# Optimization experiments

Measured on AMD Instinct MI355X. Metric: run time of the kernel, lower is better.

Reference implementation:

```python
import math
import jax, jax.numpy as jnp
import numpy as np

FEAT = (32, 96, 96)   # feature-space D,H,W (image 128x384x384 at scale 4)
C_IN = 256
DIM = 48              # patch_dim
PS = 24               # patch_size = instance_crop_size // feature_scale
SIG = 1024
POS = (8, 8, 8, 4)    # pos_emb_shape
N = 64                # num instances
SCALE = 4
CROP = 96


def setup_inputs() -> dict:
    key = jax.random.key(0)
    ks = jax.random.split(key, 16)
    def w(k, shape, s=0.02):
        return jax.random.normal(k, shape, dtype=jnp.float32) * s
    feature = jax.random.normal(ks[0], FEAT + (C_IN,), dtype=jnp.float32)
    # locations in original-image pixel coordinates
    locations = jax.random.uniform(ks[1], (N, 3), dtype=jnp.float32) * jnp.asarray(
        [FEAT[0] * SCALE, FEAT[1] * SCALE, FEAT[2] * SCALE], jnp.float32)
    return dict(
        feature=feature, locations=locations,
        conv0_w=w(ks[2], (3, 3, 3, C_IN, DIM)), conv0_b=jnp.zeros((DIM,), jnp.float32),
        conv1_w=w(ks[3], (3, 3, 3, DIM, DIM)), conv1_b=jnp.zeros((DIM,), jnp.float32),
        ca_w=w(ks[4], (DIM, DIM)), ca_b=jnp.zeros((DIM,), jnp.float32),
        sig_w=w(ks[5], (4 * 4 * 4 * DIM, SIG)), sig_b=jnp.zeros((SIG,), jnp.float32),
        ln_scale=jnp.ones((SIG,), jnp.float32), ln_bias=jnp.zeros((SIG,), jnp.float32),
        pe1_w=w(ks[6], (SIG, SIG)), pe1_b=jnp.zeros((SIG,), jnp.float32),
        pe2_w=w(ks[7], (SIG, SIG)), pe2_b=jnp.zeros((SIG,), jnp.float32),
        pe3_w=w(ks[8], (SIG, math.prod(POS))), pe3_b=jnp.zeros((math.prod(POS),), jnp.float32),
        pe_proj_w=w(ks[9], (POS[-1], DIM)),
        ct_w=w(ks[10], (2, 2, 2, DIM, 1)), ct_b=jnp.zeros((1,), jnp.float32),
    )


def _conv3d(x, w, b):
    y = jax.lax.conv_general_dilated(x[None], w, (1, 1, 1), 'SAME',
        dimension_numbers=('NDHWC', 'DHWIO', 'NDHWC'))[0]
    return y + b


def _forward(feature, locations, conv0_w, conv0_b, conv1_w, conv1_b, ca_w, ca_b,
             sig_w, sig_b, ln_scale, ln_bias, pe1_w, pe1_b, pe2_w, pe2_b,
             pe3_w, pe3_b, pe_proj_w, ct_w, ct_b):
    n = locations.shape[0]
    locs = locations / SCALE
    # feature mixing convs
    x = jax.nn.gelu(_conv3d(feature, conv0_w, conv0_b))
    x = _conv3d(x, conv1_w, conv1_b)                       # [D,H,W,DIM]
    # _get_patch: gather PS^3 sub-volumes at N locations with bounds masking
    loc0 = locs.astype(jnp.int32) - PS // 2                 # [N,3] top-left corners
    grid = jnp.mgrid[:PS, :PS, :PS]                         # [3,PS,PS,PS]
    coords = grid[None] + loc0[:, :, None, None, None]      # [N,3,PS,PS,PS]
    limit = jnp.asarray(x.shape[:-1]).reshape(1, 3, 1, 1, 1)
    valid = (coords >= 0).all(axis=1) & (coords < limit).all(axis=1)  # [N,PS,PS,PS]
    patches = jnp.where(valid[..., None],
                        x[coords[:, 0], coords[:, 1], coords[:, 2]], 0.0)
    # ChannelAttention (SE-style: global pool -> dense -> sigmoid gate)
    gate = jax.nn.sigmoid(patches.mean(axis=(1, 2, 3)) @ ca_w + ca_b)  # [N,DIM]
    patches = patches * gate[:, None, None, None, :]
    # _get_signiture
    bw = PS // 4
    inner = patches[:, bw:-bw, bw:-bw, bw:-bw, :]
    s = jax.image.resize(inner, (n, 4, 4, 4, DIM), 'linear').reshape(n, -1)
    s = s @ sig_w + sig_b
    mu = s.mean(-1, keepdims=True)
    var = ((s - mu) ** 2).mean(-1, keepdims=True)
    patch_sigs = (s - mu) * jax.lax.rsqrt(var + 1e-6) * ln_scale + ln_bias
    # _add_pos_encoding
    p = jax.nn.gelu(patch_sigs @ pe1_w + pe1_b)
    p = jax.nn.gelu(p @ pe2_w + pe2_b)
    p = p @ pe3_w + pe3_b                                   # [N, prod(POS)]
    p = jax.image.resize(p.reshape(-1, *POS), (n, PS, PS, PS, POS[-1]), 'linear')
    patches = jax.nn.relu(patches + p @ pe_proj_w)          # [N,PS,PS,PS,DIM]
    # decode: ConvTranspose x2 then trilinear resize to full crop
    logits = jax.lax.conv_transpose(patches, ct_w, (2, 2, 2), 'SAME',
        dimension_numbers=('NDHWC', 'DHWIO', 'NDHWC')) + ct_b  # [N,2PS,2PS,2PS,1]
    logits = jax.image.resize(logits[..., 0], (n, CROP, CROP, CROP), 'linear')
    mask = locs[:, -1] >= 0
    plocs = jnp.where(mask[:, None], loc0 * SCALE, -1)
    return patch_sigs, logits, plocs[:, 0], plocs[:, 1], plocs[:, 2], mask


def reference(feature, locations, conv0_w, conv0_b, conv1_w, conv1_b, ca_w, ca_b,
              sig_w, sig_b, ln_scale, ln_bias, pe1_w, pe1_b, pe2_w, pe2_b,
              pe3_w, pe3_b, pe_proj_w, ct_w, ct_b):
    return _forward(feature, locations, conv0_w, conv0_b, conv1_w, conv1_b, ca_w,
                    ca_b, sig_w, sig_b, ln_scale, ln_bias, pe1_w, pe1_b, pe2_w,
                    pe2_b, pe3_w, pe3_b, pe_proj_w, ct_w, ct_b)
```

## Files before the change

kernel.cpp:

```cpp
#include <hip/hip_runtime.h>
#include <hip/hip_bf16.h>
#include <math.h>


#define NLOC 64

typedef __attribute__((ext_vector_type(8))) short short8_t;
typedef __attribute__((ext_vector_type(4))) float f32x4;

__device__ __forceinline__ float gelu_f(float x) {
    return 0.5f * x * (1.0f + tanhf(0.7978845608028654f * (x + 0.044715f * x * x * x)));
}

__device__ __forceinline__ short f2bf(float x) {
    union { __hip_bfloat16 h; short s; } u;
    u.h = __float2bfloat16(x);
    return u.s;
}

__device__ __forceinline__ float bf2f(short s) {
    union { unsigned u; float f; } u;
    u.u = ((unsigned)(unsigned short)s) << 16;
    return u.f;
}

__constant__ float W12c[4][12] = {
    {0.25f, 0.375f, 0.25f, 0.125f, 0.f, 0.f, 0.f, 0.f, 0.f, 0.f, 0.f, 0.f},
    {0.f, 0.f, 1.f/9.f, 2.f/9.f, 1.f/3.f, 2.f/9.f, 1.f/9.f, 0.f, 0.f, 0.f, 0.f, 0.f},
    {0.f, 0.f, 0.f, 0.f, 0.f, 1.f/9.f, 2.f/9.f, 1.f/3.f, 2.f/9.f, 1.f/9.f, 0.f, 0.f},
    {0.f, 0.f, 0.f, 0.f, 0.f, 0.f, 0.f, 0.f, 0.125f, 0.25f, 0.375f, 0.25f}};

__device__ __forceinline__ void up_w(int i, float ratio, int inmax,
                                     int& j0, int& j1, float& w0, float& w1) {
    float c = ((float)i + 0.5f) * ratio - 0.5f;
    float fj = floorf(c);
    float f = c - fj;
    int jj = (int)fj;
    j0 = min(max(jj, 0), inmax);
    j1 = min(max(jj + 1, 0), inmax);
    w0 = 1.f - f;
    w1 = f;
}

__global__ void prep_w0_kernel(const float* __restrict__ w0, short* __restrict__ wf) {
    const int tid = blockIdx.x * 256 + threadIdx.x;
    if (tid >= 27 * 8 * 3 * 64) return;
    const int lane = tid & 63;
    const int t2 = tid >> 6;
    const int nt = t2 % 3;
    const int t3 = t2 / 3;
    const int kk = t3 & 7, tap = t3 >> 3;
    const int g = lane >> 4, rr = lane & 15;
    const int co = nt * 16 + rr;
    short8_t frag;
#pragma unroll
    for (int e = 0; e < 8; e++) {
        const int ci = kk * 32 + g * 8 + e;
        frag[e] = f2bf(w0[((long)(tap * 256 + ci)) * 48 + co]);
    }
    ((short8_t*)wf)[tid] = frag;
}

__global__ void prep_w1_kernel(const float* __restrict__ w1, short* __restrict__ wf) {
    const int tid = blockIdx.x * 256 + threadIdx.x;
    if (tid >= 27 * 2 * 3 * 64) return;
    const int lane = tid & 63;
    const int t2 = tid >> 6;
    const int nt = t2 % 3;
    const int t3 = t2 / 3;
    const int kk = t3 & 1, tap = t3 >> 1;
    const int g = lane >> 4, rr = lane & 15;
    const int co = nt * 16 + rr;
    short8_t frag;
#pragma unroll
    for (int e = 0; e < 8; e++) {
        const int ci = kk * 32 + g * 8 + e;
        frag[e] = (ci < 48) ? f2bf(w1[((long)(tap * 48 + ci)) * 48 + co]) : (short)0;
    }
    ((short8_t*)wf)[tid] = frag;
}

#define HV 600
#define HSTR 40

__global__ __launch_bounds__(256) void conv0_mfma(const float* __restrict__ feat,
                                                  const short* __restrict__ wf,
                                                  const float* __restrict__ bias,
                                                  short* __restrict__ x0b) {
    __shared__ short slds[HV * HSTR];
    const int tid = threadIdx.x;
    const int lane = tid & 63, wid = tid >> 6;
    const int g = lane >> 4, r = lane & 15;
    const int bz = blockIdx.x / 144, by = (blockIdx.x / 12) % 12, bx = blockIdx.x % 12;
    const int z0 = bz * 4, y0 = by * 8, x0c = bx * 8;
    int h0[4];
#pragma unroll
    for (int mt = 0; mt < 4; mt++) {
        const int t = wid * 64 + mt * 16 + r;
        h0[mt] = ((t >> 6) * 10 + ((t >> 3) & 7)) * 10 + (t & 7);
    }
    f32x4 acc[4][3];
#pragma unroll
    for (int mt = 0; mt < 4; mt++)
#pragma unroll
        for (int nt = 0; nt < 3; nt++) acc[mt][nt] = (f32x4){0.f, 0.f, 0.f, 0.f};
    const short8_t zfrag = {0, 0, 0, 0, 0, 0, 0, 0};
    const short8_t* wf8 = (const short8_t*)wf;

    for (int kk = 0; kk < 8; kk++) {
        __syncthreads();
        for (int h = tid; h < HV; h += 256) {
            const int hx = h % 10, hy = (h / 10) % 10, hz = h / 100;
            const int zz = z0 + hz - 1, yy = y0 + hy - 1, xx = x0c + hx - 1;
            short8_t s8[4];
            if ((unsigned)zz < 32u && (unsigned)yy < 96u && (unsigned)xx < 96u) {
                const float4* src =
                    (const float4*)(feat + (((((long)zz * 96 + yy) * 96 + xx)) << 8) + kk * 32);
#pragma unroll
                for (int q = 0; q < 4; q++) {
                    const float4 a = src[2 * q], b = src[2 * q + 1];
                    s8[q][0] = f2bf(a.x); s8[q][1] = f2bf(a.y);
                    s8[q][2] = f2bf(a.z); s8[q][3] = f2bf(a.w);
                    s8[q][4] = f2bf(b.x); s8[q][5] = f2bf(b.y);
                    s8[q][6] = f2bf(b.z); s8[q][7] = f2bf(b.w);
                }
            } else {
#pragma unroll
                for (int q = 0; q < 4; q++) s8[q] = zfrag;
            }
            short8_t* dst = (short8_t*)(slds + h * HSTR);
#pragma unroll
            for (int q = 0; q < 4; q++) dst[q] = s8[q];
        }
        __syncthreads();
        for (int tap = 0; tap < 27; tap++) {
            const int dh = (tap / 9) * 100 + ((tap / 3) % 3) * 10 + (tap % 3);
            short8_t bfr[3];
#pragma unroll
            for (int nt = 0; nt < 3; nt++)
                bfr[nt] = wf8[(size_t)tap * 1536 + kk * 192 + nt * 64 + lane];
            short8_t afr[4];
#pragma unroll
            for (int mt = 0; mt < 4; mt++)
                afr[mt] = *(const short8_t*)(slds + (h0[mt] + dh) * HSTR + g * 8);
#pragma unroll
            for (int mt = 0; mt < 4; mt++)
#pragma unroll
                for (int nt = 0; nt < 3; nt++)
                    acc[mt][nt] = __builtin_amdgcn_mfma_f32_16x16x32_bf16(afr[mt], bfr[nt],
                                                                          acc[mt][nt], 0, 0, 0);
        }
    }
#pragma unroll
    for (int nt = 0; nt < 3; nt++) {
        const int co = nt * 16 + r;
        const float bv = bias[co];
#pragma unroll
        for (int mt = 0; mt < 4; mt++) {
#pragma unroll
            for (int rg = 0; rg < 4; rg++) {
                const int t = wid * 64 + mt * 16 + g * 4 + rg;
                const int z = z0 + (t >> 6), y = y0 + ((t >> 3) & 7), x = x0c + (t & 7);
                const long gi = ((long)z * 96 + y) * 96 + x;
                x0b[gi * 48 + co] = f2bf(gelu_f(acc[mt][nt][rg] + bv));
            }
        }
    }
}

#define C1ROW 48

__global__ __launch_bounds__(256, 1) void conv1_mfma_b(const short* __restrict__ x0b,
                                                       const short* __restrict__ wf,
                                                       const float* __restrict__ bias,
                                                       short* __restrict__ x1b) {
    __shared__ short slds[HV * C1ROW];
    const int tid = threadIdx.x;
    const int lane = tid & 63, wid = tid >> 6;
    const int g = lane >> 4, r = lane & 15;
    const int bz = blockIdx.x / 144, by = (blockIdx.x / 12) % 12, bx = blockIdx.x % 12;
    const int z0 = bz * 4, y0 = by * 8, x0c = bx * 8;
    int h0[4];
#pragma unroll
    for (int mt = 0; mt < 4; mt++) {
        const int t = wid * 64 + mt * 16 + r;
        h0[mt] = ((t >> 6) * 10 + ((t >> 3) & 7)) * 10 + (t & 7);
    }
    f32x4 acc[4][3];
#pragma unroll
    for (int mt = 0; mt < 4; mt++)
#pragma unroll
        for (int nt = 0; nt < 3; nt++) acc[mt][nt] = (f32x4){0.f, 0.f, 0.f, 0.f};
    const short8_t zfrag = {0, 0, 0, 0, 0, 0, 0, 0};
    const short8_t* wf8 = (const short8_t*)wf;

    for (int h = tid; h < HV; h += 256) {
        const int hx = h % 10, hy = (h / 10) % 10, hz = h / 100;
        const int zz = z0 + hz - 1, yy = y0 + hy - 1, xx = x0c + hx - 1;
        short8_t s8[6];
        if ((unsigned)zz < 32u && (unsigned)yy < 96u && (unsigned)xx < 96u) {
            const short8_t* src = (const short8_t*)(x0b + (((long)zz * 96 + yy) * 96 + xx) * 48);
#pragma unroll
            for (int q = 0; q < 6; q++) s8[q] = src[q];
        } else {
#pragma unroll
            for (int q = 0; q < 6; q++) s8[q] = zfrag;
        }
        short8_t* dst = (short8_t*)(slds + h * C1ROW);
#pragma unroll
        for (int q = 0; q < 6; q++) dst[q] = s8[q];
    }
    __syncthreads();

    for (int tap = 0; tap < 27; tap++) {
        const int dh = (tap / 9) * 100 + ((tap / 3) % 3) * 10 + (tap % 3);
#pragma unroll
        for (int kk = 0; kk < 2; kk++) {
            short8_t bfr[3];
#pragma unroll
            for (int nt = 0; nt < 3; nt++)
                bfr[nt] = wf8[(size_t)tap * 384 + kk * 192 + nt * 64 + lane];
            short8_t afr[4];
#pragma unroll
            for (int mt = 0; mt < 4; mt++) {
                afr[mt] = zfrag;
                if (!(kk == 1 && g >= 2))
                    afr[mt] =
                        *(const short8_t*)(slds + (h0[mt] + dh) * C1ROW + kk * 32 + g * 8);
            }
#pragma unroll
            for (int mt = 0; mt < 4; mt++)
#pragma unroll
                for (int nt = 0; nt < 3; nt++)
                    acc[mt][nt] = __builtin_amdgcn_mfma_f32_16x16x32_bf16(afr[mt], bfr[nt],
                                                                          acc[mt][nt], 0, 0, 0);
        }
    }
#pragma unroll
    for (int nt = 0; nt < 3; nt++) {
        const int co = nt * 16 + r;
        const float bv = bias[co];
#pragma unroll
        for (int mt = 0; mt < 4; mt++) {
#pragma unroll
            for (int rg = 0; rg < 4; rg++) {
                const int t = wid * 64 + mt * 16 + g * 4 + rg;
                const int z = z0 + (t >> 6), y = y0 + ((t >> 3) & 7), x = x0c + (t & 7);
                const long gi = ((long)z * 96 + y) * 96 + x;
                x1b[gi * 48 + co] = f2bf(acc[mt][nt][rg] + bv);
            }
        }
    }
}

__global__ __launch_bounds__(256) void mean_part_kernel(const short* __restrict__ x1b,
                                                        const float* __restrict__ locations,
                                                        float* __restrict__ part) {
    __shared__ float red[256];
    const int n = blockIdx.x, i = blockIdx.y;
    const int tid = threadIdx.x;
    const int ch = tid & 63, grp = tid >> 6;
    const int lz = (int)(locations[n * 3 + 0] * 0.25f) - 12;
    const int ly = (int)(locations[n * 3 + 1] * 0.25f) - 12;
    const int lx = (int)(locations[n * 3 + 2] * 0.25f) - 12;
    float acc = 0.f;
    const int z = lz + i;
    if (ch < 48 && (unsigned)z < 32u) {
        for (int p = grp; p < 576; p += 4) {
            const int j = p / 24, k = p % 24;
            const int y = ly + j, x = lx + k;
            if ((unsigned)y < 96u && (unsigned)x < 96u)
                acc += bf2f(x1b[(((long)z * 96 + y) * 96 + x) * 48 + ch]);
        }
    }
    red[tid] = acc;
    __syncthreads();
    if (tid < 48)
        part[(n * 24 + i) * 48 + tid] = red[tid] + red[tid + 64] + red[tid + 128] + red[tid + 192];
}

__global__ void gate_kernel(const float* __restrict__ part, const float* __restrict__ caw,
                            const float* __restrict__ cab, float* __restrict__ gate) {
    __shared__ float sm[48];
    const int n = blockIdx.x, t = threadIdx.x;
    if (t < 48) {
        float a = 0.f;
        for (int i = 0; i < 24; i++) a += part[(n * 24 + i) * 48 + t];
        sm[t] = a * (1.f / 13824.f);
    }
    __syncthreads();
    if (t < 48) {
        float g = cab[t];
        for (int c = 0; c < 48; c++) g += sm[c] * caw[c * 48 + t];
        gate[n * 48 + t] = 1.f / (1.f + expf(-g));
    }
}

__global__ __launch_bounds__(256) void rs1_kernel(const short* __restrict__ x1b,
                                                  const float* __restrict__ locations,
                                                  const float* __restrict__ gate,
                                                  float* __restrict__ t1) {
    const int idx = blockIdx.x * 256 + threadIdx.x;
    int ch = idx % 48;
    int r = idx / 48;
    int c4 = r & 3; r >>= 2;
    int j = r % 12; r /= 12;
    int i = r % 12;
    int n = r / 12;
    const int lz = (int)(locations[n * 3 + 0] * 0.25f) - 6;
    const int ly = (int)(locations[n * 3 + 1] * 0.25f) - 6;
    const int lx = (int)(locations[n * 3 + 2] * 0.25f) - 6;
    const int z = lz + i, y = ly + j;
    float acc = 0.f;
    if ((unsigned)z < 32u && (unsigned)y < 96u) {
        const short* row = x1b + (((long)z * 96 + y) * 96) * 48 + ch;
#pragma unroll
        for (int k = 0; k < 12; k++) {
            const int x = lx + k;
            if ((unsigned)x < 96u) acc += W12c[c4][k] * bf2f(row[(long)x * 48]);
        }
    }
    t1[idx] = acc * gate[n * 48 + ch];
}

__global__ __launch_bounds__(256) void rs2_kernel(const float* __restrict__ t1,
                                                  float* __restrict__ t2) {
    const int idx = blockIdx.x * 256 + threadIdx.x;
    int ch = idx % 48;
    int r = idx / 48;
    int c = r & 3; r >>= 2;
    int b = r & 3; r >>= 2;
    int i = r % 12;
    int n = r / 12;
    float acc = 0.f;
#pragma unroll
    for (int j = 0; j < 12; j++)
        acc += W12c[b][j] * t1[(((long)((n * 12 + i) * 12 + j) * 4 + c)) * 48 + ch];
    t2[idx] = acc;
}

__global__ __launch_bounds__(256) void rs3_kernel(const float* __restrict__ t2,
                                                  float* __restrict__ rs) {
    const int idx = blockIdx.x * 256 + threadIdx.x;
    int ch = idx % 48;
    int r = idx / 48;
    int c = r & 3; r >>= 2;
    int b = r & 3; r >>= 2;
    int a = r & 3;
    int n = r >> 2;
    float acc = 0.f;
#pragma unroll
    for (int i = 0; i < 12; i++)
        acc += W12c[a][i] * t2[(((long)((n * 12 + i) * 4 + b) * 4 + c)) * 48 + ch];
    rs[idx] = acc;
}

template <int K, bool GEL>
__global__ __launch_bounds__(256) void mlp_kernel(const float* __restrict__ A,
                                                  const float* __restrict__ W,
                                                  const float* __restrict__ bias,
                                                  float* __restrict__ C, int N) {
    const int n = threadIdx.x & 63;
    const int j = blockIdx.x * 4 + (threadIdx.x >> 6);
    float acc = bias[j];
    const float* a = A + (long)n * K;
    const float* wp = W + j;
    for (int k = 0; k < K; k++) acc += a[k] * wp[(long)k * N];
    if (GEL) acc = gelu_f(acc);
    C[(long)n * N + j] = acc;
}

__global__ __launch_bounds__(256) void ln_kernel(const float* __restrict__ s,
                                                 const float* __restrict__ sc,
                                                 const float* __restrict__ bi,
                                                 float* __restrict__ out) {
    __shared__ float red[256];
    const int n = blockIdx.x, tid = threadIdx.x;
    float4 v = ((const float4*)(s + (long)n * 1024))[tid];
    red[tid] = v.x + v.y + v.z + v.w;
    __syncthreads();
    for (int off = 128; off > 0; off >>= 1) {
        if (tid < off) red[tid] += red[tid + off];
        __syncthreads();
    }
    const float mu = red[0] * (1.f / 1024.f);
    __syncthreads();
    const float d0 = v.x - mu, d1 = v.y - mu, d2 = v.z - mu, d3 = v.w - mu;
    red[tid] = d0 * d0 + d1 * d1 + d2 * d2 + d3 * d3;
    __syncthreads();
    for (int off = 128; off > 0; off >>= 1) {
        if (tid < off) red[tid] += red[tid + off];
        __syncthreads();
    }
    const float rstd = rsqrtf(red[0] * (1.f / 1024.f) + 1e-6f);
    const int base = n * 1024 + tid * 4;
    out[base + 0] = d0 * rstd * sc[tid * 4 + 0] + bi[tid * 4 + 0];
    out[base + 1] = d1 * rstd * sc[tid * 4 + 1] + bi[tid * 4 + 1];
    out[base + 2] = d2 * rstd * sc[tid * 4 + 2] + bi[tid * 4 + 2];
    out[base + 3] = d3 * rstd * sc[tid * 4 + 3] + bi[tid * 4 + 3];
}

__global__ __launch_bounds__(256) void deconv_kernel(const short* __restrict__ x1b,
                                                     const float* __restrict__ locations,
                                                     const float* __restrict__ gate,
                                                     const float* __restrict__ p3,
                                                     const float* __restrict__ projw,
                                                     const float* __restrict__ ctw,
                                                     const float* __restrict__ ctb,
                                                     float* __restrict__ l48) {
    __shared__ float s_ctw[384], s_proj[192], s_gate[48];
    const int n = blockIdx.y, tid = threadIdx.x;
    for (int i = tid; i < 384; i += 256) s_ctw[i] = ctw[i];
    if (tid < 192) s_proj[tid] = projw[tid];
    if (tid < 48) s_gate[tid] = gate[n * 48 + tid];
    __syncthreads();
    const int vox = blockIdx.x * 256 + tid;
    const int q = vox % 24, pp = (vox / 24) % 24, m = vox / 576;
    const int lz = (int)(locations[n * 3 + 0] * 0.25f) - 12;
    const int ly = (int)(locations[n * 3 + 1] * 0.25f) - 12;
    const int lx = (int)(locations[n * 3 + 2] * 0.25f) - 12;
    const int z = lz + m, y = ly + pp, x = lx + q;
    float pf[48];
    const bool valid = (unsigned)z < 32u && (unsigned)y < 96u && (unsigned)x < 96u;
    if (valid) {
        const short8_t* src = (const short8_t*)(x1b + (((long)z * 96 + y) * 96 + x) * 48);
#pragma unroll
        for (int t8 = 0; t8 < 6; t8++) {
            const short8_t v = src[t8];
#pragma unroll
            for (int e = 0; e < 8; e++) pf[t8 * 8 + e] = bf2f(v[e]) * s_gate[t8 * 8 + e];
        }
    } else {
#pragma unroll
        for (int c = 0; c < 48; c++) pf[c] = 0.f;
    }
    int jz[2], jy[2], jx[2];
    float wz[2], wy[2], wx[2];
    const float r3 = 1.f / 3.f;
    up_w(m, r3, 7, jz[0], jz[1], wz[0], wz[1]);
    up_w(pp, r3, 7, jy[0], jy[1], wy[0], wy[1]);
    up_w(q, r3, 7, jx[0], jx[1], wx[0], wx[1]);
    const float4* prow = (const float4*)(p3 + (long)n * 2048);
    float prx = 0.f, pry = 0.f, prz = 0.f, prw = 0.f;
#pragma unroll
    for (int a = 0; a < 2; a++)
#pragma unroll
        for (int b = 0; b < 2; b++)
#pragma unroll
            for (int c = 0; c < 2; c++) {
                const float wgt = wz[a] * wy[b] * wx[c];
                float4 v = prow[(jz[a] * 8 + jy[b]) * 8 + jx[c]];
                prx += wgt * v.x;
                pry += wgt * v.y;
                prz += wgt * v.z;
                prw += wgt * v.w;
            }
#pragma unroll
    for (int c = 0; c < 48; c++) {
        float v = pf[c] + prx * s_proj[c] + pry * s_proj[48 + c] + prz * s_proj[96 + c] +
                  prw * s_proj[144 + c];
        pf[c] = fmaxf(v, 0.f);
    }
    const float bias = ctb[0];
#pragma unroll
    for (int a = 0; a < 2; a++)
#pragma unroll
        for (int b = 0; b < 2; b++)
#pragma unroll
            for (int c = 0; c < 2; c++) {
                const float* wrow = s_ctw + (((1 - a) * 2 + (1 - b)) * 2 + (1 - c)) * 48;
                float acc = bias;
#pragma unroll
                for (int ch = 0; ch < 48; ch++) acc += pf[ch] * wrow[ch];
                l48[(((long)n * 48 + 2 * m + a) * 48 + 2 * pp + b) * 48 + 2 * q + c] = acc;
            }
}

__global__ __launch_bounds__(256) void resize96_kernel(const float* __restrict__ l48,
                                                       float* __restrict__ out) {
    const int n = blockIdx.y;
    const int vox = blockIdx.x * 256 + threadIdx.x;
    const int kx = vox % 96, jy = (vox / 96) % 96, iz = vox / 9216;
    int a0, a1, b0, b1, c0, c1;
    float wa0, wa1, wb0, wb1, wc0, wc1;
    up_w(iz, 0.5f, 47, a0, a1, wa0, wa1);
    up_w(jy, 0.5f, 47, b0, b1, wb0, wb1);
    up_w(kx, 0.5f, 47, c0, c1, wc0, wc1);
    const float* base = l48 + (long)n * 110592;
    const float v =
        wa0 * (wb0 * (wc0 * base[(a0 * 48 + b0) * 48 + c0] + wc1 * base[(a0 * 48 + b0) * 48 + c1]) +
               wb1 * (wc0 * base[(a0 * 48 + b1) * 48 + c0] + wc1 * base[(a0 * 48 + b1) * 48 + c1])) +
        wa1 * (wb0 * (wc0 * base[(a1 * 48 + b0) * 48 + c0] + wc1 * base[(a1 * 48 + b0) * 48 + c1]) +
               wb1 * (wc0 * base[(a1 * 48 + b1) * 48 + c0] + wc1 * base[(a1 * 48 + b1) * 48 + c1]));
    out[(long)n * 884736 + vox] = v;
}

__global__ void tail_kernel(const float* __restrict__ locations, float* __restrict__ out) {
    const int n = threadIdx.x;
    if (n < NLOC) {
        const float l0 = locations[n * 3 + 0] * 0.25f;
        const float l1 = locations[n * 3 + 1] * 0.25f;
        const float l2 = locations[n * 3 + 2] * 0.25f;
        const int z = (int)l0 - 12, y = (int)l1 - 12, x = (int)l2 - 12;
        const bool mask = (l2 >= 0.f);
        out[n] = mask ? (float)(z * 4) : -1.f;
        out[64 + n] = mask ? (float)(y * 4) : -1.f;
        out[128 + n] = mask ? (float)(x * 4) : -1.f;
        out[192 + n] = mask ? 1.f : 0.f;
    }
}

static const size_t OFF_X0 = 0;
static const size_t OFF_X1 = 14155776;
static const size_t OFF_WF0 = 14155776;
static const size_t OFF_GATE = 4096;
static const size_t OFF_T1 = 8192;
static const size_t OFF_T2 = 1777664;
static const size_t OFF_RS = 2367488;
static const size_t OFF_S = 2564096;
static const size_t OFF_P1 = 2629632;
static const size_t OFF_P2 = 2695168;
static const size_t OFF_P3 = 2760704;
static const size_t OFF_L48 = 2891776;
static const size_t OFF_PART = 10000000;

static const size_t OUT_WF1 = 65536;

extern "C" void kernel_launch(void* const* d_in, const int* in_sizes, int n_in,
                              void* d_out, int out_size, void* d_ws, size_t ws_size,
                              hipStream_t stream) {
    const float* feature = (const float*)d_in[0];
    const float* locations = (const float*)d_in[1];
    const float* w0 = (const float*)d_in[2];
    const float* b0 = (const float*)d_in[3];
    const float* w1 = (const float*)d_in[4];
    const float* b1 = (const float*)d_in[5];
    const float* caw = (const float*)d_in[6];
    const float* cab = (const float*)d_in[7];
    const float* sigw = (const float*)d_in[8];
    const float* sigb = (const float*)d_in[9];
    const float* lnsc = (const float*)d_in[10];
    const float* lnbi = (const float*)d_in[11];
    const float* pe1w = (const float*)d_in[12];
    const float* pe1b = (const float*)d_in[13];
    const float* pe2w = (const float*)d_in[14];
    const float* pe2b = (const float*)d_in[15];
    const float* pe3w = (const float*)d_in[16];
    const float* pe3b = (const float*)d_in[17];
    const float* projw = (const float*)d_in[18];
    const float* ctw = (const float*)d_in[19];
    const float* ctb = (const float*)d_in[20];
    float* ws = (float*)d_ws;
    float* out = (float*)d_out;

    short* x0b = (short*)(ws + OFF_X0);
    short* x1b = (short*)(ws + OFF_X1);
    short* wf0 = (short*)(ws + OFF_WF0);
    short* wf1 = (short*)(out + OUT_WF1);

    prep_w0_kernel<<<162, 256, 0, stream>>>(w0, wf0);
    prep_w1_kernel<<<41, 256, 0, stream>>>(w1, wf1);

    conv0_mfma<<<1152, 256, 0, stream>>>(feature, wf0, b0, x0b);
    conv1_mfma_b<<<1152, 256, 0, stream>>>(x0b, wf1, b1, x1b);

    mean_part_kernel<<<dim3(64, 24), 256, 0, stream>>>(x1b, locations, ws + OFF_PART);
    gate_kernel<<<64, 64, 0, stream>>>(ws + OFF_PART, caw, cab, ws + OFF_GATE);

    rs1_kernel<<<6912, 256, 0, stream>>>(x1b, locations, ws + OFF_GATE, ws + OFF_T1);
    rs2_kernel<<<2304, 256, 0, stream>>>(ws + OFF_T1, ws + OFF_T2);
    rs3_kernel<<<768, 256, 0, stream>>>(ws + OFF_T2, ws + OFF_RS);

    mlp_kernel<3072, false><<<256, 256, 0, stream>>>(ws + OFF_RS, sigw, sigb, ws + OFF_S, 1024);
    ln_kernel<<<64, 256, 0, stream>>>(ws + OFF_S, lnsc, lnbi, out);

    mlp_kernel<1024, true><<<256, 256, 0, stream>>>(out, pe1w, pe1b, ws + OFF_P1, 1024);
    mlp_kernel<1024, true><<<256, 256, 0, stream>>>(ws + OFF_P1, pe2w, pe2b, ws + OFF_P2, 1024);
    mlp_kernel<1024, false><<<512, 256, 0, stream>>>(ws + OFF_P2, pe3w, pe3b, ws + OFF_P3, 2048);

    deconv_kernel<<<dim3(54, 64), 256, 0, stream>>>(x1b, locations, ws + OFF_GATE, ws + OFF_P3,
                                                    projw, ctw, ctb, ws + OFF_L48);

    resize96_kernel<<<dim3(3456, 64), 256, 0, stream>>>(ws + OFF_L48, out + 65536);

    tail_kernel<<<1, 64, 0, stream>>>(locations, out + 56688640);
}
```

Baseline: 1.235 ms.

## Pre-cast feature to bf16 and compute conv0 directly from global memory

A separate kernel first converts the whole fp32 feature volume to bf16 in a scratch region of the output buffer. conv0 then drops its LDS halo tiling and reads MFMA A-fragments straight from the bf16 volume per tap, using a flat voxel-linear mapping instead of 4x8x8 spatial tiles. This removes the repeated fp32->bf16 conversion of halo data and the block barriers. In exchange it adds a full extra pass over the feature tensor and 27x re-reads from global/L2 without LDS reuse. It also uses the output buffer as scratch, which could conflict if that region overlaps real outputs.

Measured after the change: 1.690 ms. 1.37x slower.

```diff
diff --git a/kernel.cpp b/kernel.cpp
--- a/kernel.cpp
+++ b/kernel.cpp
@@ -6,6 +6,7 @@
 #define NLOC 64
 
 typedef __attribute__((ext_vector_type(8))) short short8_t;
+typedef __attribute__((ext_vector_type(4))) short short4_t;
 typedef __attribute__((ext_vector_type(4))) float f32x4;
 
 __device__ __forceinline__ float gelu_f(float x) {
@@ -40,6 +41,21 @@
     j1 = min(max(jj + 1, 0), inmax);
     w0 = 1.f - f;
     w1 = f;
+}
+
+__global__ __launch_bounds__(256) void cast_bf16_kernel(const float* __restrict__ in,
+                                                        short* __restrict__ o, long n4) {
+    long idx = (long)blockIdx.x * 256 + threadIdx.x;
+    const long stride = (long)gridDim.x * 256;
+    for (long i = idx; i < n4; i += stride) {
+        const float4 v = ((const float4*)in)[i];
+        short4_t s;
+        s.x = f2bf(v.x);
+        s.y = f2bf(v.y);
+        s.z = f2bf(v.z);
+        s.w = f2bf(v.w);
+        ((short4_t*)o)[i] = s;
+    }
 }
 
 __global__ void prep_w0_kernel(const float* __restrict__ w0, short* __restrict__ wf) {
@@ -80,24 +96,21 @@
     ((short8_t*)wf)[tid] = frag;
 }
 
-#define HV 600
-#define HSTR 40
-
-__global__ __launch_bounds__(256) void conv0_mfma(const float* __restrict__ feat,
-                                                  const short* __restrict__ wf,
-                                                  const float* __restrict__ bias,
-                                                  short* __restrict__ x0b) {
-    __shared__ short slds[HV * HSTR];
-    const int tid = threadIdx.x;
-    const int lane = tid & 63, wid = tid >> 6;
+__global__ __launch_bounds__(256) void conv0_direct(const short* __restrict__ featb,
+                                                    const short* __restrict__ wf,
+                                                    const float* __restrict__ bias,
+                                                    short* __restrict__ x0b) {
+    const int lane = threadIdx.x & 63;
+    const int wid = threadIdx.x >> 6;
     const int g = lane >> 4, r = lane & 15;
-    const int bz = blockIdx.x / 144, by = (blockIdx.x / 12) % 12, bx = blockIdx.x % 12;
-    const int z0 = bz * 4, y0 = by * 8, x0c = bx * 8;
-    int h0[4];
+    const int vbase = blockIdx.x * 256 + wid * 64;
+    int vx[4], vy[4], vz[4];
 #pragma unroll
     for (int mt = 0; mt < 4; mt++) {
-        const int t = wid * 64 + mt * 16 + r;
-        h0[mt] = ((t >> 6) * 10 + ((t >> 3) & 7)) * 10 + (t & 7);
+        const int v = vbase + mt * 16 + r;
+        vx[mt] = v % 96;
+        vy[mt] = (v / 96) % 96;
+        vz[mt] = v / 9216;
     }
     f32x4 acc[4][3];
 #pragma unroll
@@ -107,42 +120,25 @@
     const short8_t zfrag = {0, 0, 0, 0, 0, 0, 0, 0};
     const short8_t* wf8 = (const short8_t*)wf;
 
-    for (int kk = 0; kk < 8; kk++) {
-        __syncthreads();
-        for (int h = tid; h < HV; h += 256) {
-            const int hx = h % 10, hy = (h / 10) % 10, hz = h / 100;
-            const int zz = z0 + hz - 1, yy = y0 + hy - 1, xx = x0c + hx - 1;
-            short8_t s8[4];
-            if ((unsigned)zz < 32u && (unsigned)yy < 96u && (unsigned)xx < 96u) {
-                const float4* src =
-                    (const float4*)(feat + (((((long)zz * 96 + yy) * 96 + xx)) << 8) + kk * 32);
-#pragma unroll
-                for (int q = 0; q < 4; q++) {
-                    const float4 a = src[2 * q], b = src[2 * q + 1];
-                    s8[q][0] = f2bf(a.x); s8[q][1] = f2bf(a.y);
-                    s8[q][2] = f2bf(a.z); s8[q][3] = f2bf(a.w);
-                    s8[q][4] = f2bf(b.x); s8[q][5] = f2bf(b.y);
-                    s8[q][6] = f2bf(b.z); s8[q][7] = f2bf(b.w);
-                }
-            } else {
-#pragma unroll
-                for (int q = 0; q < 4; q++) s8[q] = zfrag;
-            }
-            short8_t* dst = (short8_t*)(slds + h * HSTR);
-#pragma unroll
-            for (int q = 0; q < 4; q++) dst[q] = s8[q];
-        }
-        __syncthreads();
-        for (int tap = 0; tap < 27; tap++) {
-            const int dh = (tap / 9) * 100 + ((tap / 3) % 3) * 10 + (tap % 3);
+    for (int tap = 0; tap < 27; tap++) {
+        const int dz = tap / 9 - 1, dy = (tap / 3) % 3 - 1, dxx = tap % 3 - 1;
+        long aoff[4];
+        bool val[4];
+#pragma unroll
+        for (int mt = 0; mt < 4; mt++) {
+            const int zz = vz[mt] + dz, yy = vy[mt] + dy, xx = vx[mt] + dxx;
+            val[mt] = ((unsigned)zz < 32u) && ((unsigned)yy < 96u) && ((unsigned)xx < 96u);
+            aoff[mt] = ((((long)zz * 96 + yy) * 96 + xx) << 8) + g * 8;
+        }
+        const short8_t* bp = wf8 + (size_t)tap * 1536 + lane;
+        for (int kk = 0; kk < 8; kk++) {
             short8_t bfr[3];
 #pragma unroll
-            for (int nt = 0; nt < 3; nt++)
-                bfr[nt] = wf8[(size_t)tap * 1536 + kk * 192 + nt * 64 + lane];
+            for (int nt = 0; nt < 3; nt++) bfr[nt] = bp[kk * 192 + nt * 64];
             short8_t afr[4];
 #pragma unroll
             for (int mt = 0; mt < 4; mt++)
-                afr[mt] = *(const short8_t*)(slds + (h0[mt] + dh) * HSTR + g * 8);
+                afr[mt] = val[mt] ? *(const short8_t*)(featb + aoff[mt] + kk * 32) : zfrag;
 #pragma unroll
             for (int mt = 0; mt < 4; mt++)
 #pragma unroll
@@ -157,17 +153,15 @@
         const float bv = bias[co];
 #pragma unroll
         for (int mt = 0; mt < 4; mt++) {
-#pragma unroll
-            for (int rg = 0; rg < 4; rg++) {
-                const int t = wid * 64 + mt * 16 + g * 4 + rg;
-                const int z = z0 + (t >> 6), y = y0 + ((t >> 3) & 7), x = x0c + (t & 7);
-                const long gi = ((long)z * 96 + y) * 96 + x;
-                x0b[gi * 48 + co] = f2bf(gelu_f(acc[mt][nt][rg] + bv));
-            }
-        }
-    }
-}
-
+            const int vox = vbase + mt * 16 + g * 4;
+#pragma unroll
+            for (int rg = 0; rg < 4; rg++)
+                x0b[(long)(vox + rg) * 48 + co] = f2bf(gelu_f(acc[mt][nt][rg] + bv));
+        }
+    }
+}
+
+#define HV 600
 #define C1ROW 48
 
 __global__ __launch_bounds__(256, 1) void conv1_mfma_b(const short* __restrict__ x0b,
@@ -512,7 +506,8 @@
 
 static const size_t OFF_X0 = 0;
 static const size_t OFF_X1 = 14155776;
-static const size_t OFF_WF0 = 14155776;
+static const size_t OFF_WF0 = 14155776 + 7077888;
+static const size_t OFF_WF0R = 17694720;
 static const size_t OFF_GATE = 4096;
 static const size_t OFF_T1 = 8192;
 static const size_t OFF_T2 = 1777664;
@@ -525,6 +520,7 @@
 static const size_t OFF_PART = 10000000;
 
 static const size_t OUT_WF1 = 65536;
+static const size_t OUT_FEATB = 200000;
 
 extern "C" void kernel_launch(void* const* d_in, const int* in_sizes, int n_in,
                               void* d_out, int out_size, void* d_ws, size_t ws_size,
@@ -555,13 +551,15 @@
 
     short* x0b = (short*)(ws + OFF_X0);
     short* x1b = (short*)(ws + OFF_X1);
-    short* wf0 = (short*)(ws + OFF_WF0);
+    short* wf0 = (short*)(ws + OFF_WF0R);
     short* wf1 = (short*)(out + OUT_WF1);
-
+    short* featb = (short*)(out + OUT_FEATB);
+
+    cast_bf16_kernel<<<4096, 256, 0, stream>>>(feature, featb, 75497472L / 4);
     prep_w0_kernel<<<162, 256, 0, stream>>>(w0, wf0);
     prep_w1_kernel<<<41, 256, 0, stream>>>(w1, wf1);
 
-    conv0_mfma<<<1152, 256, 0, stream>>>(feature, wf0, b0, x0b);
+    conv0_direct<<<1152, 256, 0, stream>>>(featb, wf0, b0, x0b);
     conv1_mfma_b<<<1152, 256, 0, stream>>>(x0b, wf1, b1, x1b);
 
     mean_part_kernel<<<dim3(64, 24), 256, 0, stream>>>(x1b, locations, ws + OFF_PART);
```
